# Performance work log

Hardware: AMD Instinct MI355X
Metric: run time of the kernel (lower is better)

Reference implementation:

```python
import jax, jax.numpy as jnp
import numpy as np
import math

DIM = 256
B, H, W = 8, 64, 64


def setup_inputs() -> dict:
    key = jax.random.key(0)
    ks = jax.random.split(key, 8)
    d4 = DIM // 4
    s = 1.0 / math.sqrt(DIM)
    return {
        "sem": jax.random.normal(ks[0], (B, DIM, H, W), jnp.float32),
        "foren": jax.random.normal(ks[1], (B, DIM, H, W), jnp.float32),
        "Wq": jax.random.normal(ks[2], (d4, DIM), jnp.float32) * s,
        "bq": jnp.zeros((d4,), jnp.float32),
        "Wk": jax.random.normal(ks[3], (d4, DIM), jnp.float32) * s,
        "bk": jnp.zeros((d4,), jnp.float32),
        "Wv": jax.random.normal(ks[4], (DIM, DIM), jnp.float32) * s,
        "bv": jnp.zeros((DIM,), jnp.float32),
        "gamma": jnp.zeros((1,), jnp.float32),
    }


def reference(sem, foren, Wq, bq, Wk, bk, Wv, bv, gamma):
    Bn, C, Hn, Wn = sem.shape
    HW = Hn * Wn
    # 1x1 convs == per-pixel linear projections
    q = jnp.einsum('oc,bchw->bohw', Wq, sem) + bq[None, :, None, None]
    k = jnp.einsum('oc,bchw->bohw', Wk, foren) + bk[None, :, None, None]
    v = jnp.einsum('oc,bchw->bohw', Wv, foren) + bv[None, :, None, None]
    q = q.reshape(Bn, -1, HW).transpose(0, 2, 1)        # [B, HW, C/4]
    k = k.reshape(Bn, -1, HW)                           # [B, C/4, HW]
    v = v.reshape(Bn, C, HW)                            # [B, C, HW]
    attn = jnp.einsum('bnd,bdm->bnm', q, k) / math.sqrt(C // 4)
    attn = jax.nn.softmax(attn, axis=-1)                # [B, HW, HW]
    out = jnp.einsum('bcm,bnm->bcn', v, attn).reshape(Bn, C, Hn, Wn)
    return sem + gamma * out
```

## Files before the change

### kernel.cpp

```cpp
#include <hip/hip_runtime.h>
#include <stdint.h>

typedef unsigned short u16;
typedef unsigned int u32;
typedef short s16x8 __attribute__((ext_vector_type(8)));
typedef float f32x4 __attribute__((ext_vector_type(4)));
typedef float f32x16 __attribute__((ext_vector_type(16)));
typedef u32 u32x2 __attribute__((ext_vector_type(2)));

#define DIM 256
#define HW  4096
#define NB  8
#define QSCL 0.18033688011112042f

template <int N> struct ic { static constexpr int value = N; };

__device__ __forceinline__ u16 f2bf(float f) {
  union { float f; unsigned u; } v; v.f = f;
  unsigned r = v.u + 0x7FFFu + ((v.u >> 16) & 1u);
  return (u16)(r >> 16);
}
__device__ __forceinline__ float fexp2(float x) { return __builtin_amdgcn_exp2f(x); }

typedef __attribute__((address_space(1))) const void gvoid_c;
typedef __attribute__((address_space(3))) void lvoid;
__device__ __forceinline__ void gload_lds16(const void* g, void* l) {
  __builtin_amdgcn_global_load_lds((gvoid_c*)g, (lvoid*)l, 16, 0, 0);
}
__device__ __forceinline__ f32x16 mfma32(s16x8 a, s16x8 b, f32x16 c) {
  return __builtin_amdgcn_mfma_f32_32x32x16_bf16(a, b, c, 0, 0, 0);
}
__device__ __forceinline__ f32x4 mfma16(s16x8 a, s16x8 b, f32x4 c) {
  return __builtin_amdgcn_mfma_f32_16x16x32_bf16(a, b, c, 0, 0, 0);
}

__global__ void prep_w(const float* __restrict__ Wq, const float* __restrict__ Wk,
                       const float* __restrict__ Wv, u16* __restrict__ dst,
                       u32* __restrict__ knmax_u) {
  int idx = blockIdx.x * 256 + threadIdx.x;
  if (blockIdx.x == 0 && threadIdx.x < 8) knmax_u[threadIdx.x] = 0u;
  float v;
  if (idx < 16384)        v = Wq[idx] * QSCL;
  else if (idx < 32768)   v = Wk[idx - 16384];
  else                    v = Wv[idx - 32768];
  dst[idx] = f2bf(v);
}

__global__ __launch_bounds__(256) void proj_q(
    const float* __restrict__ sem, const u16* __restrict__ Wqb, const float* __restrict__ bq,
    u16* __restrict__ Qo, float* __restrict__ qnsq) {
  __shared__ u16 lds[16384];
  const int t = threadIdx.x, b = blockIdx.x & 7, n0 = (blockIdx.x >> 3) * 64;
  {
    const int px = t & 63, cb = (t >> 6) * 8, swz = (px & 31) * 8;
    for (int i = 0; i < 8; ++i) {
      int c0 = i * 32 + cb;
      size_t gb = ((size_t)b * DIM + c0) * HW + n0 + px;
      s16x8 us;
#pragma unroll
      for (int j = 0; j < 8; ++j) us[j] = (short)f2bf(sem[gb + (size_t)j * HW]);
      *(s16x8*)(lds + px * 256 + (c0 ^ swz)) = us;
    }
  }
  __syncthreads();
  const int w = t >> 6, lane = t & 63, l15 = lane & 15, g = lane >> 4;
  const int px = w * 16 + l15;
  s16x8 bx[8];
#pragma unroll
  for (int kc = 0; kc < 8; ++kc)
    bx[kc] = *(const s16x8*)(lds + px * 256 + (((kc * 4 + g) ^ (px & 31)) * 8));
  float nrm = 0.f;
#pragma unroll
  for (int ct = 0; ct < 4; ++ct) {
    f32x4 bb = *(const f32x4*)(bq + ct * 16 + 4 * g);
    f32x4 acc;
#pragma unroll
    for (int j = 0; j < 4; ++j) acc[j] = bb[j] * QSCL;
#pragma unroll
    for (int kc = 0; kc < 8; ++kc) {
      s16x8 aw = *(const s16x8*)(Wqb + (ct * 16 + l15) * 256 + kc * 32 + g * 8);
      acc = mfma16(aw, bx[kc], acc);
    }
    u32 lo = (u32)f2bf(acc[0]) | ((u32)f2bf(acc[1]) << 16);
    u32 hi = (u32)f2bf(acc[2]) | ((u32)f2bf(acc[3]) << 16);
    u32x2 pk; pk[0] = lo; pk[1] = hi;
    *(u32x2*)(Qo + ((size_t)b * HW + n0 + px) * 64 + ct * 16 + 4 * g) = pk;
#pragma unroll
    for (int j = 0; j < 4; ++j) nrm += acc[j] * acc[j];
  }
  nrm += __shfl_xor(nrm, 16);
  nrm += __shfl_xor(nrm, 32);
  if (g == 0) qnsq[(size_t)b * HW + n0 + px] = nrm;
}

__global__ __launch_bounds__(256) void proj_kv(
    const float* __restrict__ foren, const u16* __restrict__ Wkb, const u16* __restrict__ Wvb,
    const float* __restrict__ bk, const float* __restrict__ bv,
    u16* __restrict__ Ko, u16* __restrict__ Vo, u32* __restrict__ knmax_u) {
  __shared__ u16 lds[16384];
  const int t = threadIdx.x, b = blockIdx.x & 7, n0 = (blockIdx.x >> 3) * 64;
  {
    const int px = t & 63, cb = (t >> 6) * 8, swz = (px & 31) * 8;
    for (int i = 0; i < 8; ++i) {
      int c0 = i * 32 + cb;
      size_t gb = ((size_t)b * DIM + c0) * HW + n0 + px;
      s16x8 uf;
#pragma unroll
      for (int j = 0; j < 8; ++j) uf[j] = (short)f2bf(foren[gb + (size_t)j * HW]);
      *(s16x8*)(lds + px * 256 + (c0 ^ swz)) = uf;
    }
  }
  __syncthreads();
  const int w = t >> 6, lane = t & 63, l15 = lane & 15, g = lane >> 4;
  {
    const int px = w * 16 + l15;
    s16x8 bx[8];
#pragma unroll
    for (int kc = 0; kc < 8; ++kc)
      bx[kc] = *(const s16x8*)(lds + px * 256 + (((kc * 4 + g) ^ (px & 31)) * 8));
    float nrm = 0.f;
#pragma unroll
    for (int ct = 0; ct < 4; ++ct) {
      f32x4 acc = *(const f32x4*)(bk + ct * 16 + 4 * g);
#pragma unroll
      for (int kc = 0; kc < 8; ++kc) {
        s16x8 aw = *(const s16x8*)(Wkb + (ct * 16 + l15) * 256 + kc * 32 + g * 8);
        acc = mfma16(aw, bx[kc], acc);
      }
      u32 lo = (u32)f2bf(acc[0]) | ((u32)f2bf(acc[1]) << 16);
      u32 hi = (u32)f2bf(acc[2]) | ((u32)f2bf(acc[3]) << 16);
      u32x2 pk; pk[0] = lo; pk[1] = hi;
      *(u32x2*)(Ko + ((size_t)b * HW + n0 + px) * 64 + ct * 16 + 4 * g) = pk;
#pragma unroll
      for (int j = 0; j < 4; ++j) nrm += acc[j] * acc[j];
    }
    nrm += __shfl_xor(nrm, 16);
    nrm += __shfl_xor(nrm, 32);
    nrm = fmaxf(nrm, __shfl_xor(nrm, 1));
    nrm = fmaxf(nrm, __shfl_xor(nrm, 2));
    nrm = fmaxf(nrm, __shfl_xor(nrm, 4));
    nrm = fmaxf(nrm, __shfl_xor(nrm, 8));
    if (lane == 0) atomicMax(knmax_u + b, __float_as_uint(nrm));
  }
#pragma unroll
  for (int ct2 = 0; ct2 < 4; ++ct2) {
    const int c0 = w * 64 + ct2 * 16;
    s16x8 aw[8];
#pragma unroll
    for (int kc = 0; kc < 8; ++kc)
      aw[kc] = *(const s16x8*)(Wvb + (c0 + l15) * 256 + kc * 32 + g * 8);
#pragma unroll
    for (int pxt = 0; pxt < 4; ++pxt) {
      const int px = pxt * 16 + l15;
      f32x4 acc = *(const f32x4*)(bv + c0 + 4 * g);
#pragma unroll
      for (int kc = 0; kc < 8; ++kc) {
        s16x8 bxp = *(const s16x8*)(lds + px * 256 + (((kc * 4 + g) ^ (px & 31)) * 8));
        acc = mfma16(aw[kc], bxp, acc);
      }
#pragma unroll
      for (int j = 0; j < 4; ++j)
        Vo[((size_t)b * DIM + c0 + 4 * g + j) * HW + n0 + pxt * 16 + l15] = f2bf(acc[j]);
    }
  }
}

__global__ __launch_bounds__(512, 1) void attn3(
    const u16* __restrict__ Qg, const u16* __restrict__ Kg, const u16* __restrict__ Vg,
    const float* __restrict__ qnsq, const u32* __restrict__ knmax_u,
    const float* __restrict__ sem, const float* __restrict__ gamma_p,
    float* __restrict__ out) {
  __shared__ u16 lds[49664];
  char* ldsb = (char*)lds;
  const int t = threadIdx.x;
  const int b = blockIdx.x & 7;
  const int n0 = (blockIdx.x >> 3) << 7;
  const int w = t >> 6, lane = t & 63;
  const int l31 = lane & 31, g5 = lane >> 5;

  const u16* Qb = Qg + (size_t)b * HW * 64;
  const u16* Kb = Kg + (size_t)b * HW * 64;
  const u16* Vb = Vg + (size_t)b * DIM * HW;

  const int hh = w >> 2, rr = w & 3;
  const int key0 = hh * 32 + l31;
  const int qrow = rr * 32 + l31;
  int ka[4];
#pragma unroll
  for (int ks = 0; ks < 4; ++ks)
    ka[ks] = key0 * 128 + (((ks * 2 + g5) ^ (key0 & 7)) * 16);
  s16x8 qb[4];
#pragma unroll
  for (int ks = 0; ks < 4; ++ks)
    qb[ks] = *(const s16x8*)(Qb + (size_t)(n0 + qrow) * 64 + ks * 16 + g5 * 8);
  int pw_[4];
#pragma unroll
  for (int jg = 0; jg < 4; ++jg)
    pw_[jg] = 81920 + qrow * 128 + (((hh * 4 + jg) ^ (qrow & 7)) * 16) + g5 * 8;
  const float mr = sqrtf(qnsq[(size_t)b * HW + n0 + qrow] * __uint_as_float(knmax_u[b])) * 1.02f;

  const int rw = w >> 2, cw = w & 3;
  int pa[2][4], va[2][4];
#pragma unroll
  for (int rt = 0; rt < 2; ++rt)
#pragma unroll
    for (int ks = 0; ks < 4; ++ks) {
      int r = rw * 64 + rt * 32 + l31;
      pa[rt][ks] = 81920 + r * 128 + (((ks * 2 + g5) ^ (r & 7)) * 16);
    }
#pragma unroll
  for (int ct = 0; ct < 2; ++ct)
#pragma unroll
    for (int ks = 0; ks < 4; ++ks) {
      int c = cw * 64 + ct * 32 + l31;
      va[ct][ks] = 16384 + c * 128 + (((ks * 2 + g5) ^ (c & 7)) * 16);
    }

  f32x16 O[4] = {};
  float lreg = 0.f;

  const int srow = lane >> 3;
  const int sx = ((lane & 7) ^ srow) * 8;

  auto STAGE = [&](int buf, int kt) {
    const u16* ksrc = Kb + ((size_t)(kt * 64 + w * 8 + srow)) * 64 + sx;
    gload_lds16(ksrc, (void*)(lds + buf * 4096 + w * 512));
#pragma unroll
    for (int i = 0; i < 4; ++i) {
      int c = (i * 8 + w) * 8 + srow;
      const u16* vsrc = Vb + (size_t)c * HW + kt * 64 + sx;
      gload_lds16(vsrc, (void*)(lds + 8192 + buf * 16384 + (i * 8 + w) * 512));
    }
  };

  auto tile = [&](auto BUFC, int kt, bool dostage) {
    constexpr int BUF = decltype(BUFC)::value;
    if (dostage) STAGE(BUF ^ 1, kt + 1);
    f32x16 sc = {};
#pragma unroll
    for (int ks = 0; ks < 4; ++ks) {
      s16x8 ak = *(const s16x8*)(ldsb + ka[ks] + BUF * 8192);
      sc = mfma32(ak, qb[ks], sc);
    }
#pragma unroll
    for (int jg = 0; jg < 4; ++jg) {
      float p0 = fexp2(sc[jg * 4 + 0] - mr);
      float p1 = fexp2(sc[jg * 4 + 1] - mr);
      float p2 = fexp2(sc[jg * 4 + 2] - mr);
      float p3 = fexp2(sc[jg * 4 + 3] - mr);
      lreg += (p0 + p1) + (p2 + p3);
      u32 w0, w1;
      asm("v_cvt_pk_bf16_f32 %0, %1, %2" : "=v"(w0) : "v"(p0), "v"(p1));
      asm("v_cvt_pk_bf16_f32 %0, %1, %2" : "=v"(w1) : "v"(p2), "v"(p3));
      u32x2 pk; pk[0] = w0; pk[1] = w1;
      *(u32x2*)(ldsb + pw_[jg]) = pk;
    }
    asm volatile("s_waitcnt lgkmcnt(0)" ::: "memory");
    __builtin_amdgcn_s_barrier();
    __builtin_amdgcn_sched_barrier(0);
#pragma unroll
    for (int ks = 0; ks < 4; ++ks) {
      s16x8 ap0 = *(const s16x8*)(ldsb + pa[0][ks]);
      s16x8 ap1 = *(const s16x8*)(ldsb + pa[1][ks]);
      s16x8 vb0 = *(const s16x8*)(ldsb + va[0][ks] + BUF * 32768);
      s16x8 vb1 = *(const s16x8*)(ldsb + va[1][ks] + BUF * 32768);
      O[0] = mfma32(ap0, vb0, O[0]);
      O[1] = mfma32(ap0, vb1, O[1]);
      O[2] = mfma32(ap1, vb0, O[2]);
      O[3] = mfma32(ap1, vb1, O[3]);
    }
    __syncthreads();
  };

  STAGE(0, 0);
  __syncthreads();
  for (int kt = 0; kt < 64; kt += 2) {
    tile(ic<0>{}, kt, true);
    tile(ic<1>{}, kt + 1, kt + 2 < 64);
  }

  float* lfp = (float*)(ldsb + 98304);
  float ls = lreg + __shfl_xor(lreg, 32);
  if (lane < 32) lfp[hh * 128 + qrow] = ls;
  __syncthreads();
  const float gm = gamma_p[0];
#pragma unroll
  for (int rt = 0; rt < 2; ++rt) {
#pragma unroll
    for (int jg = 0; jg < 4; ++jg) {
      const int noff = rw * 64 + rt * 32 + jg * 8 + 4 * g5;
      f32x4 l0 = *(const f32x4*)(lfp + noff);
      f32x4 l1 = *(const f32x4*)(lfp + 128 + noff);
      f32x4 inv;
#pragma unroll
      for (int j = 0; j < 4; ++j) inv[j] = __builtin_amdgcn_rcpf(l0[j] + l1[j]);
#pragma unroll
      for (int ct = 0; ct < 2; ++ct) {
        const int c = cw * 64 + ct * 32 + l31;
        size_t base = ((size_t)b * DIM + c) * HW + n0 + noff;
        f32x4 sv = *(const f32x4*)(sem + base);
        f32x4 ov;
#pragma unroll
        for (int j = 0; j < 4; ++j)
          ov[j] = sv[j] + gm * (O[rt * 2 + ct][jg * 4 + j] * inv[j]);
        *(f32x4*)(out + base) = ov;
      }
    }
  }
}

extern "C" void kernel_launch(void* const* d_in, const int* in_sizes, int n_in,
                              void* d_out, int out_size, void* d_ws, size_t ws_size,
                              hipStream_t stream) {
  const float* sem   = (const float*)d_in[0];
  const float* foren = (const float*)d_in[1];
  const float* Wq    = (const float*)d_in[2];
  const float* bq    = (const float*)d_in[3];
  const float* Wk    = (const float*)d_in[4];
  const float* bk    = (const float*)d_in[5];
  const float* Wv    = (const float*)d_in[6];
  const float* bv    = (const float*)d_in[7];
  const float* gamma = (const float*)d_in[8];
  float* out = (float*)d_out;

  u16* Wqb = (u16*)d_ws;
  u16* Wkb = Wqb + 16384;
  u16* Wvb = Wkb + 16384;
  u16* Q   = Wvb + 65536;
  u16* K   = Q + (size_t)NB * HW * 64;
  u16* V   = K + (size_t)NB * HW * 64;
  float* qnsq = (float*)(V + (size_t)NB * DIM * HW);
  u32* knmax_u = (u32*)(qnsq + (size_t)NB * HW);

  prep_w <<<384, 256, 0, stream>>>(Wq, Wk, Wv, Wqb, knmax_u);
  proj_q <<<512, 256, 0, stream>>>(sem, Wqb, bq, Q, qnsq);
  proj_kv<<<512, 256, 0, stream>>>(foren, Wkb, Wvb, bk, bv, K, V, knmax_u);
  attn3  <<<256, 512, 0, stream>>>(Q, K, V, qnsq, knmax_u, sem, gamma, out);
}
```

Measured before the change: 166.3 us.

## Specialize attention warps into producer/consumer roles and merge projection kernels

```diff
diff --git a/kernel.cpp b/kernel.cpp
--- a/kernel.cpp
+++ b/kernel.cpp
@@ -46,11 +46,17 @@
   dst[idx] = f2bf(v);
 }
 
-__global__ __launch_bounds__(256) void proj_q(
-    const float* __restrict__ sem, const u16* __restrict__ Wqb, const float* __restrict__ bq,
-    u16* __restrict__ Qo, float* __restrict__ qnsq) {
+__global__ __launch_bounds__(256) void proj_all(
+    const float* __restrict__ sem, const float* __restrict__ foren,
+    const u16* __restrict__ Wqb, const u16* __restrict__ Wkb, const u16* __restrict__ Wvb,
+    const float* __restrict__ bq, const float* __restrict__ bk, const float* __restrict__ bv,
+    u16* __restrict__ Qo, u16* __restrict__ Ko, u16* __restrict__ Vo,
+    float* __restrict__ qnsq, u32* __restrict__ knmax_u) {
   __shared__ u16 lds[16384];
-  const int t = threadIdx.x, b = blockIdx.x & 7, n0 = (blockIdx.x >> 3) * 64;
+  const bool qpath = blockIdx.x < 512;
+  const int bid = qpath ? blockIdx.x : blockIdx.x - 512;
+  const int t = threadIdx.x, b = bid & 7, n0 = (bid >> 3) * 64;
+  const float* X = qpath ? sem : foren;
   {
     const int px = t & 63, cb = (t >> 6) * 8, swz = (px & 31) * 8;
     for (int i = 0; i < 8; ++i) {
@@ -58,60 +64,43 @@
       size_t gb = ((size_t)b * DIM + c0) * HW + n0 + px;
       s16x8 us;
 #pragma unroll
-      for (int j = 0; j < 8; ++j) us[j] = (short)f2bf(sem[gb + (size_t)j * HW]);
+      for (int j = 0; j < 8; ++j) us[j] = (short)f2bf(X[gb + (size_t)j * HW]);
       *(s16x8*)(lds + px * 256 + (c0 ^ swz)) = us;
     }
   }
   __syncthreads();
   const int w = t >> 6, lane = t & 63, l15 = lane & 15, g = lane >> 4;
-  const int px = w * 16 + l15;
-  s16x8 bx[8];
-#pragma unroll
-  for (int kc = 0; kc < 8; ++kc)
-    bx[kc] = *(const s16x8*)(lds + px * 256 + (((kc * 4 + g) ^ (px & 31)) * 8));
-  float nrm = 0.f;
-#pragma unroll
-  for (int ct = 0; ct < 4; ++ct) {
-    f32x4 bb = *(const f32x4*)(bq + ct * 16 + 4 * g);
-    f32x4 acc;
-#pragma unroll
-    for (int j = 0; j < 4; ++j) acc[j] = bb[j] * QSCL;
-#pragma unroll
-    for (int kc = 0; kc < 8; ++kc) {
-      s16x8 aw = *(const s16x8*)(Wqb + (ct * 16 + l15) * 256 + kc * 32 + g * 8);
-      acc = mfma16(aw, bx[kc], acc);
-    }
-    u32 lo = (u32)f2bf(acc[0]) | ((u32)f2bf(acc[1]) << 16);
-    u32 hi = (u32)f2bf(acc[2]) | ((u32)f2bf(acc[3]) << 16);
-    u32x2 pk; pk[0] = lo; pk[1] = hi;
-    *(u32x2*)(Qo + ((size_t)b * HW + n0 + px) * 64 + ct * 16 + 4 * g) = pk;
-#pragma unroll
-    for (int j = 0; j < 4; ++j) nrm += acc[j] * acc[j];
-  }
-  nrm += __shfl_xor(nrm, 16);
-  nrm += __shfl_xor(nrm, 32);
-  if (g == 0) qnsq[(size_t)b * HW + n0 + px] = nrm;
-}
-
-__global__ __launch_bounds__(256) void proj_kv(
-    const float* __restrict__ foren, const u16* __restrict__ Wkb, const u16* __restrict__ Wvb,
-    const float* __restrict__ bk, const float* __restrict__ bv,
-    u16* __restrict__ Ko, u16* __restrict__ Vo, u32* __restrict__ knmax_u) {
-  __shared__ u16 lds[16384];
-  const int t = threadIdx.x, b = blockIdx.x & 7, n0 = (blockIdx.x >> 3) * 64;
-  {
-    const int px = t & 63, cb = (t >> 6) * 8, swz = (px & 31) * 8;
-    for (int i = 0; i < 8; ++i) {
-      int c0 = i * 32 + cb;
-      size_t gb = ((size_t)b * DIM + c0) * HW + n0 + px;
-      s16x8 uf;
-#pragma unroll
-      for (int j = 0; j < 8; ++j) uf[j] = (short)f2bf(foren[gb + (size_t)j * HW]);
-      *(s16x8*)(lds + px * 256 + (c0 ^ swz)) = uf;
-    }
-  }
-  __syncthreads();
-  const int w = t >> 6, lane = t & 63, l15 = lane & 15, g = lane >> 4;
+
+  if (qpath) {
+    const int px = w * 16 + l15;
+    s16x8 bx[8];
+#pragma unroll
+    for (int kc = 0; kc < 8; ++kc)
+      bx[kc] = *(const s16x8*)(lds + px * 256 + (((kc * 4 + g) ^ (px & 31)) * 8));
+    float nrm = 0.f;
+#pragma unroll
+    for (int ct = 0; ct < 4; ++ct) {
+      f32x4 bb = *(const f32x4*)(bq + ct * 16 + 4 * g);
+      f32x4 acc;
+#pragma unroll
+      for (int j = 0; j < 4; ++j) acc[j] = bb[j] * QSCL;
+#pragma unroll
+      for (int kc = 0; kc < 8; ++kc) {
+        s16x8 aw = *(const s16x8*)(Wqb + (ct * 16 + l15) * 256 + kc * 32 + g * 8);
+        acc = mfma16(aw, bx[kc], acc);
+      }
+      u32 lo = (u32)f2bf(acc[0]) | ((u32)f2bf(acc[1]) << 16);
+      u32 hi = (u32)f2bf(acc[2]) | ((u32)f2bf(acc[3]) << 16);
+      u32x2 pk; pk[0] = lo; pk[1] = hi;
+      *(u32x2*)(Qo + ((size_t)b * HW + n0 + px) * 64 + ct * 16 + 4 * g) = pk;
+#pragma unroll
+      for (int j = 0; j < 4; ++j) nrm += acc[j] * acc[j];
+    }
+    nrm += __shfl_xor(nrm, 16);
+    nrm += __shfl_xor(nrm, 32);
+    if (g == 0) qnsq[(size_t)b * HW + n0 + px] = nrm;
+    return;
+  }
   {
     const int px = w * 16 + l15;
     s16x8 bx[8];
@@ -165,18 +154,19 @@
   }
 }
 
-__global__ __launch_bounds__(512, 1) void attn3(
+__global__ __launch_bounds__(1024, 4) void attn4(
     const u16* __restrict__ Qg, const u16* __restrict__ Kg, const u16* __restrict__ Vg,
     const float* __restrict__ qnsq, const u32* __restrict__ knmax_u,
     const float* __restrict__ sem, const float* __restrict__ gamma_p,
     float* __restrict__ out) {
-  __shared__ u16 lds[49664];
+  __shared__ u16 lds[33280];
   char* ldsb = (char*)lds;
   const int t = threadIdx.x;
   const int b = blockIdx.x & 7;
   const int n0 = (blockIdx.x >> 3) << 7;
   const int w = t >> 6, lane = t & 63;
   const int l31 = lane & 31, g5 = lane >> 5;
+  const bool qk = w < 8;
 
   const u16* Qb = Qg + (size_t)b * HW * 64;
   const u16* Kb = Kg + (size_t)b * HW * 64;
@@ -185,126 +175,125 @@
   const int hh = w >> 2, rr = w & 3;
   const int key0 = hh * 32 + l31;
   const int qrow = rr * 32 + l31;
-  int ka[4];
-#pragma unroll
-  for (int ks = 0; ks < 4; ++ks)
-    ka[ks] = key0 * 128 + (((ks * 2 + g5) ^ (key0 & 7)) * 16);
+  int ka[4], pw_[4];
   s16x8 qb[4];
-#pragma unroll
-  for (int ks = 0; ks < 4; ++ks)
-    qb[ks] = *(const s16x8*)(Qb + (size_t)(n0 + qrow) * 64 + ks * 16 + g5 * 8);
-  int pw_[4];
-#pragma unroll
-  for (int jg = 0; jg < 4; ++jg)
-    pw_[jg] = 81920 + qrow * 128 + (((hh * 4 + jg) ^ (qrow & 7)) * 16) + g5 * 8;
-  const float mr = sqrtf(qnsq[(size_t)b * HW + n0 + qrow] * __uint_as_float(knmax_u[b])) * 1.02f;
-
-  const int rw = w >> 2, cw = w & 3;
-  int pa[2][4], va[2][4];
-#pragma unroll
-  for (int rt = 0; rt < 2; ++rt)
+  float mr = 0.f, lreg = 0.f;
+  if (qk) {
 #pragma unroll
     for (int ks = 0; ks < 4; ++ks) {
-      int r = rw * 64 + rt * 32 + l31;
-      pa[rt][ks] = 81920 + r * 128 + (((ks * 2 + g5) ^ (r & 7)) * 16);
-    }
-#pragma unroll
-  for (int ct = 0; ct < 2; ++ct)
-#pragma unroll
-    for (int ks = 0; ks < 4; ++ks) {
-      int c = cw * 64 + ct * 32 + l31;
-      va[ct][ks] = 16384 + c * 128 + (((ks * 2 + g5) ^ (c & 7)) * 16);
-    }
-
-  f32x16 O[4] = {};
-  float lreg = 0.f;
-
+      ka[ks] = key0 * 128 + (((ks * 2 + g5) ^ (key0 & 7)) * 16);
+      qb[ks] = *(const s16x8*)(Qb + (size_t)(n0 + qrow) * 64 + ks * 16 + g5 * 8);
+    }
+#pragma unroll
+    for (int jg = 0; jg < 4; ++jg)
+      pw_[jg] = 49152 + qrow * 128 + (((hh * 4 + jg) ^ (qrow & 7)) * 16) + g5 * 8;
+    mr = sqrtf(qnsq[(size_t)b * HW + n0 + qrow] * __uint_as_float(knmax_u[b])) * 1.02f;
+  }
+
+  const int w8 = w - 8;
   const int srow = lane >> 3;
   const int sx = ((lane & 7) ^ srow) * 8;
 
-  auto STAGE = [&](int buf, int kt) {
-    const u16* ksrc = Kb + ((size_t)(kt * 64 + w * 8 + srow)) * 64 + sx;
-    gload_lds16(ksrc, (void*)(lds + buf * 4096 + w * 512));
-#pragma unroll
-    for (int i = 0; i < 4; ++i) {
-      int c = (i * 8 + w) * 8 + srow;
-      const u16* vsrc = Vb + (size_t)c * HW + kt * 64 + sx;
-      gload_lds16(vsrc, (void*)(lds + 8192 + buf * 16384 + (i * 8 + w) * 512));
-    }
-  };
-
-  auto tile = [&](auto BUFC, int kt, bool dostage) {
-    constexpr int BUF = decltype(BUFC)::value;
-    if (dostage) STAGE(BUF ^ 1, kt + 1);
-    f32x16 sc = {};
-#pragma unroll
-    for (int ks = 0; ks < 4; ++ks) {
-      s16x8 ak = *(const s16x8*)(ldsb + ka[ks] + BUF * 8192);
-      sc = mfma32(ak, qb[ks], sc);
-    }
-#pragma unroll
-    for (int jg = 0; jg < 4; ++jg) {
-      float p0 = fexp2(sc[jg * 4 + 0] - mr);
-      float p1 = fexp2(sc[jg * 4 + 1] - mr);
-      float p2 = fexp2(sc[jg * 4 + 2] - mr);
-      float p3 = fexp2(sc[jg * 4 + 3] - mr);
-      lreg += (p0 + p1) + (p2 + p3);
-      u32 w0, w1;
-      asm("v_cvt_pk_bf16_f32 %0, %1, %2" : "=v"(w0) : "v"(p0), "v"(p1));
-      asm("v_cvt_pk_bf16_f32 %0, %1, %2" : "=v"(w1) : "v"(p2), "v"(p3));
-      u32x2 pk; pk[0] = w0; pk[1] = w1;
-      *(u32x2*)(ldsb + pw_[jg]) = pk;
-    }
-    asm volatile("s_waitcnt lgkmcnt(0)" ::: "memory");
+  const int rb = w & 3, cb2 = (w >> 2) & 3;
+  int pa[4], va[2][4];
+#pragma unroll
+  for (int ks = 0; ks < 4; ++ks) {
+    int r = rb * 32 + l31;
+    pa[ks] = 49152 + r * 128 + (((ks * 2 + g5) ^ (r & 7)) * 16);
+#pragma unroll
+    for (int ct = 0; ct < 2; ++ct) {
+      int c = cb2 * 64 + ct * 32 + l31;
+      va[ct][ks] = 16384 + c * 128 + (((ks * 2 + g5) ^ (c & 7)) * 16);
+    }
+  }
+  f32x16 O[2] = {};
+
+  auto tile = [&](auto KB, int kt) {
+    constexpr int KBUF = decltype(KB)::value;
+    if (qk) {
+      f32x16 sc = {};
+#pragma unroll
+      for (int ks = 0; ks < 4; ++ks) {
+        s16x8 ak = *(const s16x8*)(ldsb + ka[ks] + KBUF * 8192);
+        sc = mfma32(ak, qb[ks], sc);
+      }
+#pragma unroll
+      for (int jg = 0; jg < 4; ++jg) {
+        float p0 = fexp2(sc[jg * 4 + 0] - mr);
+        float p1 = fexp2(sc[jg * 4 + 1] - mr);
+        float p2 = fexp2(sc[jg * 4 + 2] - mr);
+        float p3 = fexp2(sc[jg * 4 + 3] - mr);
+        lreg += (p0 + p1) + (p2 + p3);
+        u32 w0, w1;
+        asm("v_cvt_pk_bf16_f32 %0, %1, %2" : "=v"(w0) : "v"(p0), "v"(p1));
+        asm("v_cvt_pk_bf16_f32 %0, %1, %2" : "=v"(w1) : "v"(p2), "v"(p3));
+        u32x2 pk; pk[0] = w0; pk[1] = w1;
+        *(u32x2*)(ldsb + pw_[jg]) = pk;
+      }
+      asm volatile("s_waitcnt lgkmcnt(0)" ::: "memory");
+    } else {
+#pragma unroll
+      for (int i = 0; i < 4; ++i) {
+        int chunk = i * 8 + w8;
+        const u16* vsrc = Vb + (size_t)(chunk * 8 + srow) * HW + kt * 64 + sx;
+        gload_lds16(vsrc, (void*)(lds + 8192 + chunk * 512));
+      }
+      {
+        const u16* ksrc = Kb + ((size_t)((kt + 1) * 64 + w8 * 8 + srow)) * 64 + sx;
+        gload_lds16(ksrc, (void*)(lds + (KBUF ^ 1) * 4096 + w8 * 512));
+      }
+      asm volatile("s_waitcnt vmcnt(1)" ::: "memory");
+    }
     __builtin_amdgcn_s_barrier();
     __builtin_amdgcn_sched_barrier(0);
+    __builtin_amdgcn_s_setprio(1);
 #pragma unroll
     for (int ks = 0; ks < 4; ++ks) {
-      s16x8 ap0 = *(const s16x8*)(ldsb + pa[0][ks]);
-      s16x8 ap1 = *(const s16x8*)(ldsb + pa[1][ks]);
-      s16x8 vb0 = *(const s16x8*)(ldsb + va[0][ks] + BUF * 32768);
-      s16x8 vb1 = *(const s16x8*)(ldsb + va[1][ks] + BUF * 32768);
-      O[0] = mfma32(ap0, vb0, O[0]);
-      O[1] = mfma32(ap0, vb1, O[1]);
-      O[2] = mfma32(ap1, vb0, O[2]);
-      O[3] = mfma32(ap1, vb1, O[3]);
-    }
+      s16x8 ap = *(const s16x8*)(ldsb + pa[ks]);
+      s16x8 v0 = *(const s16x8*)(ldsb + va[0][ks]);
+      s16x8 v1 = *(const s16x8*)(ldsb + va[1][ks]);
+      O[0] = mfma32(ap, v0, O[0]);
+      O[1] = mfma32(ap, v1, O[1]);
+    }
+    __builtin_amdgcn_s_setprio(0);
     __syncthreads();
   };
 
-  STAGE(0, 0);
+  if (!qk) {
+    const u16* ksrc = Kb + ((size_t)(w8 * 8 + srow)) * 64 + sx;
+    gload_lds16(ksrc, (void*)(lds + w8 * 512));
+  }
   __syncthreads();
   for (int kt = 0; kt < 64; kt += 2) {
-    tile(ic<0>{}, kt, true);
-    tile(ic<1>{}, kt + 1, kt + 2 < 64);
-  }
-
-  float* lfp = (float*)(ldsb + 98304);
-  float ls = lreg + __shfl_xor(lreg, 32);
-  if (lane < 32) lfp[hh * 128 + qrow] = ls;
+    tile(ic<0>{}, kt);
+    tile(ic<1>{}, kt + 1);
+  }
+
+  float* lfp = (float*)(ldsb + 65536);
+  if (qk) {
+    float ls = lreg + __shfl_xor(lreg, 32);
+    if (lane < 32) lfp[hh * 128 + qrow] = ls;
+  }
   __syncthreads();
   const float gm = gamma_p[0];
 #pragma unroll
-  for (int rt = 0; rt < 2; ++rt) {
-#pragma unroll
-    for (int jg = 0; jg < 4; ++jg) {
-      const int noff = rw * 64 + rt * 32 + jg * 8 + 4 * g5;
-      f32x4 l0 = *(const f32x4*)(lfp + noff);
-      f32x4 l1 = *(const f32x4*)(lfp + 128 + noff);
-      f32x4 inv;
-#pragma unroll
-      for (int j = 0; j < 4; ++j) inv[j] = __builtin_amdgcn_rcpf(l0[j] + l1[j]);
-#pragma unroll
-      for (int ct = 0; ct < 2; ++ct) {
-        const int c = cw * 64 + ct * 32 + l31;
-        size_t base = ((size_t)b * DIM + c) * HW + n0 + noff;
-        f32x4 sv = *(const f32x4*)(sem + base);
-        f32x4 ov;
-#pragma unroll
-        for (int j = 0; j < 4; ++j)
-          ov[j] = sv[j] + gm * (O[rt * 2 + ct][jg * 4 + j] * inv[j]);
-        *(f32x4*)(out + base) = ov;
-      }
+  for (int jg = 0; jg < 4; ++jg) {
+    const int noff = rb * 32 + jg * 8 + 4 * g5;
+    f32x4 l0 = *(const f32x4*)(lfp + noff);
+    f32x4 l1 = *(const f32x4*)(lfp + 128 + noff);
+    f32x4 inv;
+#pragma unroll
+    for (int j = 0; j < 4; ++j) inv[j] = __builtin_amdgcn_rcpf(l0[j] + l1[j]);
+#pragma unroll
+    for (int ct = 0; ct < 2; ++ct) {
+      const int c = cb2 * 64 + ct * 32 + l31;
+      size_t base = ((size_t)b * DIM + c) * HW + n0 + noff;
+      f32x4 sv = *(const f32x4*)(sem + base);
+      f32x4 ov;
+#pragma unroll
+      for (int j = 0; j < 4; ++j)
+        ov[j] = sv[j] + gm * (O[ct][jg * 4 + j] * inv[j]);
+      *(f32x4*)(out + base) = ov;
     }
   }
 }
@@ -332,8 +321,7 @@
   float* qnsq = (float*)(V + (size_t)NB * DIM * HW);
   u32* knmax_u = (u32*)(qnsq + (size_t)NB * HW);
 
-  prep_w <<<384, 256, 0, stream>>>(Wq, Wk, Wv, Wqb, knmax_u);
-  proj_q <<<512, 256, 0, stream>>>(sem, Wqb, bq, Q, qnsq);
-  proj_kv<<<512, 256, 0, stream>>>(foren, Wkb, Wvb, bk, bv, K, V, knmax_u);
-  attn3  <<<256, 512, 0, stream>>>(Q, K, V, qnsq, knmax_u, sem, gamma, out);
-}
+  prep_w  <<<384, 256, 0, stream>>>(Wq, Wk, Wv, Wqb, knmax_u);
+  proj_all<<<1024, 256, 0, stream>>>(sem, foren, Wqb, Wkb, Wvb, bq, bk, bv, Q, K, V, qnsq, knmax_u);
+  attn4   <<<256, 1024, 0, stream>>>(Q, K, V, qnsq, knmax_u, sem, gamma, out);
+}
```

Result: slower. 172.3 us (+3.6%).

## Software-pipeline attention with triple-buffered V and merge projection kernels

Applied to the files above, without the earlier changes.

```diff
diff --git a/kernel.cpp b/kernel.cpp
--- a/kernel.cpp
+++ b/kernel.cpp
@@ -21,6 +21,9 @@
   return (u16)(r >> 16);
 }
 __device__ __forceinline__ float fexp2(float x) { return __builtin_amdgcn_exp2f(x); }
+__device__ __forceinline__ u32 cvtpk(float a, float b) {
+  u32 r; asm("v_cvt_pk_bf16_f32 %0, %1, %2" : "=v"(r) : "v"(a), "v"(b)); return r;
+}
 
 typedef __attribute__((address_space(1))) const void gvoid_c;
 typedef __attribute__((address_space(3))) void lvoid;
@@ -46,11 +49,17 @@
   dst[idx] = f2bf(v);
 }
 
-__global__ __launch_bounds__(256) void proj_q(
-    const float* __restrict__ sem, const u16* __restrict__ Wqb, const float* __restrict__ bq,
-    u16* __restrict__ Qo, float* __restrict__ qnsq) {
+__global__ __launch_bounds__(256) void proj_all(
+    const float* __restrict__ sem, const float* __restrict__ foren,
+    const u16* __restrict__ Wqb, const u16* __restrict__ Wkb, const u16* __restrict__ Wvb,
+    const float* __restrict__ bq, const float* __restrict__ bk, const float* __restrict__ bv,
+    u16* __restrict__ Qo, u16* __restrict__ Ko, u16* __restrict__ Vo,
+    float* __restrict__ qnsq, u32* __restrict__ knmax_u) {
   __shared__ u16 lds[16384];
-  const int t = threadIdx.x, b = blockIdx.x & 7, n0 = (blockIdx.x >> 3) * 64;
+  const bool qpath = blockIdx.x < 512;
+  const int bid = qpath ? blockIdx.x : blockIdx.x - 512;
+  const int t = threadIdx.x, b = bid & 7, n0 = (bid >> 3) * 64;
+  const float* X = qpath ? sem : foren;
   {
     const int px = t & 63, cb = (t >> 6) * 8, swz = (px & 31) * 8;
     for (int i = 0; i < 8; ++i) {
@@ -58,60 +67,43 @@
       size_t gb = ((size_t)b * DIM + c0) * HW + n0 + px;
       s16x8 us;
 #pragma unroll
-      for (int j = 0; j < 8; ++j) us[j] = (short)f2bf(sem[gb + (size_t)j * HW]);
+      for (int j = 0; j < 8; ++j) us[j] = (short)f2bf(X[gb + (size_t)j * HW]);
       *(s16x8*)(lds + px * 256 + (c0 ^ swz)) = us;
     }
   }
   __syncthreads();
   const int w = t >> 6, lane = t & 63, l15 = lane & 15, g = lane >> 4;
-  const int px = w * 16 + l15;
-  s16x8 bx[8];
-#pragma unroll
-  for (int kc = 0; kc < 8; ++kc)
-    bx[kc] = *(const s16x8*)(lds + px * 256 + (((kc * 4 + g) ^ (px & 31)) * 8));
-  float nrm = 0.f;
-#pragma unroll
-  for (int ct = 0; ct < 4; ++ct) {
-    f32x4 bb = *(const f32x4*)(bq + ct * 16 + 4 * g);
-    f32x4 acc;
-#pragma unroll
-    for (int j = 0; j < 4; ++j) acc[j] = bb[j] * QSCL;
-#pragma unroll
-    for (int kc = 0; kc < 8; ++kc) {
-      s16x8 aw = *(const s16x8*)(Wqb + (ct * 16 + l15) * 256 + kc * 32 + g * 8);
-      acc = mfma16(aw, bx[kc], acc);
-    }
-    u32 lo = (u32)f2bf(acc[0]) | ((u32)f2bf(acc[1]) << 16);
-    u32 hi = (u32)f2bf(acc[2]) | ((u32)f2bf(acc[3]) << 16);
-    u32x2 pk; pk[0] = lo; pk[1] = hi;
-    *(u32x2*)(Qo + ((size_t)b * HW + n0 + px) * 64 + ct * 16 + 4 * g) = pk;
-#pragma unroll
-    for (int j = 0; j < 4; ++j) nrm += acc[j] * acc[j];
-  }
-  nrm += __shfl_xor(nrm, 16);
-  nrm += __shfl_xor(nrm, 32);
-  if (g == 0) qnsq[(size_t)b * HW + n0 + px] = nrm;
-}
-
-__global__ __launch_bounds__(256) void proj_kv(
-    const float* __restrict__ foren, const u16* __restrict__ Wkb, const u16* __restrict__ Wvb,
-    const float* __restrict__ bk, const float* __restrict__ bv,
-    u16* __restrict__ Ko, u16* __restrict__ Vo, u32* __restrict__ knmax_u) {
-  __shared__ u16 lds[16384];
-  const int t = threadIdx.x, b = blockIdx.x & 7, n0 = (blockIdx.x >> 3) * 64;
-  {
-    const int px = t & 63, cb = (t >> 6) * 8, swz = (px & 31) * 8;
-    for (int i = 0; i < 8; ++i) {
-      int c0 = i * 32 + cb;
-      size_t gb = ((size_t)b * DIM + c0) * HW + n0 + px;
-      s16x8 uf;
-#pragma unroll
-      for (int j = 0; j < 8; ++j) uf[j] = (short)f2bf(foren[gb + (size_t)j * HW]);
-      *(s16x8*)(lds + px * 256 + (c0 ^ swz)) = uf;
-    }
-  }
-  __syncthreads();
-  const int w = t >> 6, lane = t & 63, l15 = lane & 15, g = lane >> 4;
+
+  if (qpath) {
+    const int px = w * 16 + l15;
+    s16x8 bx[8];
+#pragma unroll
+    for (int kc = 0; kc < 8; ++kc)
+      bx[kc] = *(const s16x8*)(lds + px * 256 + (((kc * 4 + g) ^ (px & 31)) * 8));
+    float nrm = 0.f;
+#pragma unroll
+    for (int ct = 0; ct < 4; ++ct) {
+      f32x4 bb = *(const f32x4*)(bq + ct * 16 + 4 * g);
+      f32x4 acc;
+#pragma unroll
+      for (int j = 0; j < 4; ++j) acc[j] = bb[j] * QSCL;
+#pragma unroll
+      for (int kc = 0; kc < 8; ++kc) {
+        s16x8 aw = *(const s16x8*)(Wqb + (ct * 16 + l15) * 256 + kc * 32 + g * 8);
+        acc = mfma16(aw, bx[kc], acc);
+      }
+      u32 lo = (u32)f2bf(acc[0]) | ((u32)f2bf(acc[1]) << 16);
+      u32 hi = (u32)f2bf(acc[2]) | ((u32)f2bf(acc[3]) << 16);
+      u32x2 pk; pk[0] = lo; pk[1] = hi;
+      *(u32x2*)(Qo + ((size_t)b * HW + n0 + px) * 64 + ct * 16 + 4 * g) = pk;
+#pragma unroll
+      for (int j = 0; j < 4; ++j) nrm += acc[j] * acc[j];
+    }
+    nrm += __shfl_xor(nrm, 16);
+    nrm += __shfl_xor(nrm, 32);
+    if (g == 0) qnsq[(size_t)b * HW + n0 + px] = nrm;
+    return;
+  }
   {
     const int px = w * 16 + l15;
     s16x8 bx[8];
@@ -165,12 +157,12 @@
   }
 }
 
-__global__ __launch_bounds__(512, 1) void attn3(
+__global__ __launch_bounds__(512, 1) void attn11(
     const u16* __restrict__ Qg, const u16* __restrict__ Kg, const u16* __restrict__ Vg,
     const float* __restrict__ qnsq, const u32* __restrict__ knmax_u,
     const float* __restrict__ sem, const float* __restrict__ gamma_p,
     float* __restrict__ out) {
-  __shared__ u16 lds[49664];
+  __shared__ u16 lds[74240];
   char* ldsb = (char*)lds;
   const int t = threadIdx.x;
   const int b = blockIdx.x & 7;
@@ -196,8 +188,8 @@
   int pw_[4];
 #pragma unroll
   for (int jg = 0; jg < 4; ++jg)
-    pw_[jg] = 81920 + qrow * 128 + (((hh * 4 + jg) ^ (qrow & 7)) * 16) + g5 * 8;
-  const float mr = sqrtf(qnsq[(size_t)b * HW + n0 + qrow] * __uint_as_float(knmax_u[b])) * 1.02f;
+    pw_[jg] = qrow * 128 + (((hh * 4 + jg) ^ (qrow & 7)) * 16) + g5 * 8;
+  const float mneg = -(sqrtf(qnsq[(size_t)b * HW + n0 + qrow] * __uint_as_float(knmax_u[b])) * 1.02f);
 
   const int rw = w >> 2, cw = w & 3;
   int pa[2][4], va[2][4];
@@ -206,14 +198,14 @@
 #pragma unroll
     for (int ks = 0; ks < 4; ++ks) {
       int r = rw * 64 + rt * 32 + l31;
-      pa[rt][ks] = 81920 + r * 128 + (((ks * 2 + g5) ^ (r & 7)) * 16);
+      pa[rt][ks] = r * 128 + (((ks * 2 + g5) ^ (r & 7)) * 16);
     }
 #pragma unroll
   for (int ct = 0; ct < 2; ++ct)
 #pragma unroll
     for (int ks = 0; ks < 4; ++ks) {
       int c = cw * 64 + ct * 32 + l31;
-      va[ct][ks] = 16384 + c * 128 + (((ks * 2 + g5) ^ (c & 7)) * 16);
+      va[ct][ks] = 50176 + c * 128 + (((ks * 2 + g5) ^ (c & 7)) * 16);
     }
 
   f32x16 O[4] = {};
@@ -221,65 +213,105 @@
 
   const int srow = lane >> 3;
   const int sx = ((lane & 7) ^ srow) * 8;
-
-  auto STAGE = [&](int buf, int kt) {
-    const u16* ksrc = Kb + ((size_t)(kt * 64 + w * 8 + srow)) * 64 + sx;
-    gload_lds16(ksrc, (void*)(lds + buf * 4096 + w * 512));
-#pragma unroll
-    for (int i = 0; i < 4; ++i) {
-      int c = (i * 8 + w) * 8 + srow;
-      const u16* vsrc = Vb + (size_t)c * HW + kt * 64 + sx;
-      gload_lds16(vsrc, (void*)(lds + 8192 + buf * 16384 + (i * 8 + w) * 512));
-    }
-  };
-
-  auto tile = [&](auto BUFC, int kt, bool dostage) {
-    constexpr int BUF = decltype(BUFC)::value;
-    if (dostage) STAGE(BUF ^ 1, kt + 1);
-    f32x16 sc = {};
+  const u16* kp  = Kb + (size_t)(w * 8 + srow) * 64 + sx;
+  const u16* vp0 = Vb + (size_t)((0 * 8 + w) * 8 + srow) * HW + sx;
+  const u16* vp1 = Vb + (size_t)((1 * 8 + w) * 8 + srow) * HW + sx;
+  const u16* vp2 = Vb + (size_t)((2 * 8 + w) * 8 + srow) * HW + sx;
+  const u16* vp3 = Vb + (size_t)((3 * 8 + w) * 8 + srow) * HW + sx;
+
+  auto STAGE_K = [&](int dstB) {
+    gload_lds16(kp, (void*)(ldsb + dstB + w * 1024)); kp += 4096;
+  };
+  auto STAGE_V = [&](int dstB) {
+    gload_lds16(vp0, (void*)(ldsb + dstB + (0 * 8 + w) * 1024)); vp0 += 64;
+    gload_lds16(vp1, (void*)(ldsb + dstB + (1 * 8 + w) * 1024)); vp1 += 64;
+    gload_lds16(vp2, (void*)(ldsb + dstB + (2 * 8 + w) * 1024)); vp2 += 64;
+    gload_lds16(vp3, (void*)(ldsb + dstB + (3 * 8 + w) * 1024)); vp3 += 64;
+  };
+
+  auto do_qk = [&](auto KRC, auto PWC) {
+    constexpr int KR = decltype(KRC)::value;
+    constexpr int PW = decltype(PWC)::value;
+    f32x16 sc;
+#pragma unroll
+    for (int r = 0; r < 16; ++r) sc[r] = mneg;
 #pragma unroll
     for (int ks = 0; ks < 4; ++ks) {
-      s16x8 ak = *(const s16x8*)(ldsb + ka[ks] + BUF * 8192);
-      sc = mfma32(ak, qb[ks], sc);
+      s16x8 kf = *(const s16x8*)(ldsb + KR + ka[ks]);
+      sc = mfma32(kf, qb[ks], sc);
     }
 #pragma unroll
     for (int jg = 0; jg < 4; ++jg) {
-      float p0 = fexp2(sc[jg * 4 + 0] - mr);
-      float p1 = fexp2(sc[jg * 4 + 1] - mr);
-      float p2 = fexp2(sc[jg * 4 + 2] - mr);
-      float p3 = fexp2(sc[jg * 4 + 3] - mr);
+      float p0 = fexp2(sc[jg * 4 + 0]);
+      float p1 = fexp2(sc[jg * 4 + 1]);
+      float p2 = fexp2(sc[jg * 4 + 2]);
+      float p3 = fexp2(sc[jg * 4 + 3]);
       lreg += (p0 + p1) + (p2 + p3);
-      u32 w0, w1;
-      asm("v_cvt_pk_bf16_f32 %0, %1, %2" : "=v"(w0) : "v"(p0), "v"(p1));
-      asm("v_cvt_pk_bf16_f32 %0, %1, %2" : "=v"(w1) : "v"(p2), "v"(p3));
+      u32 w0 = cvtpk(p0, p1), w1 = cvtpk(p2, p3);
       u32x2 pk; pk[0] = w0; pk[1] = w1;
-      *(u32x2*)(ldsb + pw_[jg]) = pk;
-    }
-    asm volatile("s_waitcnt lgkmcnt(0)" ::: "memory");
-    __builtin_amdgcn_s_barrier();
-    __builtin_amdgcn_sched_barrier(0);
+      *(u32x2*)(ldsb + PW + pw_[jg]) = pk;
+    }
+  };
+
+  auto do_pv = [&](auto PRC) {
+    constexpr int PR = decltype(PRC)::value;
+    __builtin_amdgcn_s_setprio(1);
 #pragma unroll
     for (int ks = 0; ks < 4; ++ks) {
-      s16x8 ap0 = *(const s16x8*)(ldsb + pa[0][ks]);
-      s16x8 ap1 = *(const s16x8*)(ldsb + pa[1][ks]);
-      s16x8 vb0 = *(const s16x8*)(ldsb + va[0][ks] + BUF * 32768);
-      s16x8 vb1 = *(const s16x8*)(ldsb + va[1][ks] + BUF * 32768);
+      s16x8 ap0 = *(const s16x8*)(ldsb + PR + pa[0][ks]);
+      s16x8 ap1 = *(const s16x8*)(ldsb + PR + pa[1][ks]);
+      s16x8 vb0 = *(const s16x8*)(ldsb + va[0][ks]);
+      s16x8 vb1 = *(const s16x8*)(ldsb + va[1][ks]);
       O[0] = mfma32(ap0, vb0, O[0]);
       O[1] = mfma32(ap0, vb1, O[1]);
       O[2] = mfma32(ap1, vb0, O[2]);
       O[3] = mfma32(ap1, vb1, O[3]);
     }
-    __syncthreads();
-  };
-
-  STAGE(0, 0);
-  __syncthreads();
-  for (int kt = 0; kt < 64; kt += 2) {
-    tile(ic<0>{}, kt, true);
-    tile(ic<1>{}, kt + 1, kt + 2 < 64);
-  }
-
-  float* lfp = (float*)(ldsb + 98304);
+    __builtin_amdgcn_s_setprio(0);
+  };
+
+  auto iter = [&](auto PARC, auto VBC, bool qk_next) {
+    constexpr int PAR = decltype(PARC)::value;
+    constexpr int VB  = decltype(VBC)::value;
+    __builtin_amdgcn_s_barrier();
+    __builtin_amdgcn_sched_barrier(0);
+    STAGE_K(PAR * 8192);
+    STAGE_V(50176 + ((VB + 2) % 3) * 32768);
+    if (qk_next)
+      do_qk(ic<(PAR ^ 1) * 8192>{}, ic<16384 + (PAR ^ 1) * 16384>{});
+    do_pv(ic<16384 + PAR * 16384>{});
+    constexpr int D = (VB == 2) ? -65536 : 32768;
+#pragma unroll
+    for (int ct = 0; ct < 2; ++ct)
+#pragma unroll
+      for (int ks = 0; ks < 4; ++ks) va[ct][ks] += D;
+    asm volatile("s_waitcnt vmcnt(4) lgkmcnt(0)" ::: "memory");
+  };
+
+  STAGE_K(0);
+  STAGE_V(50176);
+  STAGE_K(8192);
+  STAGE_V(50176 + 32768);
+  asm volatile("s_waitcnt vmcnt(4)" ::: "memory");
+  __builtin_amdgcn_s_barrier();
+  __builtin_amdgcn_sched_barrier(0);
+  do_qk(ic<0>{}, ic<16384>{});
+  asm volatile("s_waitcnt lgkmcnt(0)" ::: "memory");
+
+  for (int kt = 0; kt < 60; kt += 6) {
+    iter(ic<0>{}, ic<0>{}, true);
+    iter(ic<1>{}, ic<1>{}, true);
+    iter(ic<0>{}, ic<2>{}, true);
+    iter(ic<1>{}, ic<0>{}, true);
+    iter(ic<0>{}, ic<1>{}, true);
+    iter(ic<1>{}, ic<2>{}, true);
+  }
+  iter(ic<0>{}, ic<0>{}, true);
+  iter(ic<1>{}, ic<1>{}, true);
+  iter(ic<0>{}, ic<2>{}, true);
+  iter(ic<1>{}, ic<0>{}, false);
+
+  float* lfp = (float*)(ldsb + 49152);
   float ls = lreg + __shfl_xor(lreg, 32);
   if (lane < 32) lfp[hh * 128 + qrow] = ls;
   __syncthreads();
@@ -332,8 +364,7 @@
   float* qnsq = (float*)(V + (size_t)NB * DIM * HW);
   u32* knmax_u = (u32*)(qnsq + (size_t)NB * HW);
 
-  prep_w <<<384, 256, 0, stream>>>(Wq, Wk, Wv, Wqb, knmax_u);
-  proj_q <<<512, 256, 0, stream>>>(sem, Wqb, bq, Q, qnsq);
-  proj_kv<<<512, 256, 0, stream>>>(foren, Wkb, Wvb, bk, bv, K, V, knmax_u);
-  attn3  <<<256, 512, 0, stream>>>(Q, K, V, qnsq, knmax_u, sem, gamma, out);
-}
+  prep_w  <<<384, 256, 0, stream>>>(Wq, Wk, Wv, Wqb, knmax_u);
+  proj_all<<<1024, 256, 0, stream>>>(sem, foren, Wqb, Wkb, Wvb, bq, bk, bv, Q, K, V, qnsq, knmax_u);
+  attn11  <<<256, 512, 0, stream>>>(Q, K, V, qnsq, knmax_u, sem, gamma, out);
+}
```

Result: faster. 155.8 us, median of 2 (-6.3%).
